# Kernel optimization log

Hardware: AMD Instinct MI355X
Metric: run time of the kernel (lower is better)

Reference implementation:

```python
import jax, jax.numpy as jnp
import numpy as np

B, L, D, H = 8, 1024, 512, 8
DH = D // H
DF = 2048


def setup_inputs() -> dict:
    key = jax.random.key(0)
    ks = jax.random.split(key, 13)
    s = 0.02
    return {
        "hid": jax.random.normal(ks[0], (B, L, D), jnp.float32),
        "img": jax.random.normal(ks[1], (B, L, D), jnp.float32),
        "Wq": s * jax.random.normal(ks[2], (D, D), jnp.float32),
        "Wk": s * jax.random.normal(ks[3], (D, D), jnp.float32),
        "Wv": s * jax.random.normal(ks[4], (D, D), jnp.float32),
        "Wo": s * jax.random.normal(ks[5], (D, D), jnp.float32),
        "Wq2": s * jax.random.normal(ks[6], (D, D), jnp.float32),
        "Wk2": s * jax.random.normal(ks[7], (D, D), jnp.float32),
        "Wv2": s * jax.random.normal(ks[8], (D, D), jnp.float32),
        "Wo2": s * jax.random.normal(ks[9], (D, D), jnp.float32),
        "W1": s * jax.random.normal(ks[10], (D, DF), jnp.float32),
        "W2": s * jax.random.normal(ks[11], (DF, D), jnp.float32),
        "seq": jax.random.randint(ks[12], (B, L), 0, 4),
        "SOC": 3,
        "EOS": 100,
    }


def _ln(x):
    mu = x.mean(-1, keepdims=True)
    v = x.var(-1, keepdims=True)
    return (x - mu) * jax.lax.rsqrt(v + 1e-5)


def _attn(q_in, k_in, v_in, Wq, Wk, Wv, Wo, key_mask=None):
    b, lq, _ = q_in.shape
    q = (q_in @ Wq).reshape(b, lq, H, DH)
    k = (k_in @ Wk).reshape(b, -1, H, DH)
    v = (v_in @ Wv).reshape(b, -1, H, DH)
    scores = jnp.einsum('bqhd,bkhd->bhqk', q, k) * (1.0 / np.sqrt(DH))
    if key_mask is not None:
        scores = jnp.where(key_mask[:, None, None, :], scores, jnp.float32(-1e9))
    a = jax.nn.softmax(scores, axis=-1)
    o = jnp.einsum('bhqk,bkhd->bqhd', a, v).reshape(b, lq, D)
    return o @ Wo


def reference(hid, img, Wq, Wk, Wv, Wo, Wq2, Wk2, Wv2, Wo2, W1, W2, seq, SOC, EOS):
    # cell-start mask: SOC tokens before the first EOS
    soc = (seq == SOC) & (jnp.cumsum(seq == EOS, axis=1) == 0)  # [B,L]
    # stable compaction: True positions first, original order preserved
    order = jnp.argsort(~soc, axis=1, stable=True)              # [B,L]
    ext = jnp.take_along_axis(hid, order[:, :, None], axis=1)   # [B,L,D]
    counts = soc.sum(axis=1)                                    # [B]
    run = jnp.arange(L)[None, :] < counts[:, None]              # [B,L] = extract(soc, soc)
    ext = jnp.where(run[:, :, None], ext, 0.0)                  # zero padding rows (F.pad)
    # Blocks: pre-LN masked self-attn + cross-attn to img + FFN
    x = ext
    xn = _ln(x)
    x = x + _attn(xn, xn, xn, Wq, Wk, Wv, Wo, key_mask=run)
    x = x + _attn(_ln(x), img, img, Wq2, Wk2, Wv2, Wo2)
    x = x + jax.nn.gelu(_ln(x) @ W1) @ W2
    # masked_scatter: write the first `count` rows of x back at soc positions, in order
    inv = jnp.argsort(order, axis=1)
    back = jnp.take_along_axis(x, inv[:, :, None], axis=1)
    hid_new = jnp.where(soc[:, :, None], back, hid)
    return (hid_new, x)
```

## Files before the change

kernel.cpp:

```cpp
#include <hip/hip_runtime.h>
#include <cmath>

#define B 8
#define L 1024
#define D 512
#define H 8
#define DH 64
#define DF 2048
#define BLD (B*L*D)
#define M_TOT (B*L)

typedef __attribute__((ext_vector_type(8))) short bf16x8;
typedef __attribute__((ext_vector_type(4))) float f32x4;
typedef const __attribute__((address_space(1))) void* gas_ptr;
typedef __attribute__((address_space(3))) void* las_ptr;

__device__ __forceinline__ unsigned short f2bf(float f) {
    unsigned int u = __builtin_bit_cast(unsigned int, f);
    u += 0x7FFFu + ((u >> 16) & 1u);
    return (unsigned short)(u >> 16);
}
__device__ __forceinline__ float bf2f(unsigned short s) {
    return __builtin_bit_cast(float, ((unsigned int)s) << 16);
}

__device__ __forceinline__ float gelu_f(float x) {
    float x3 = x * x * x;
    return 0.5f * x * (1.0f + tanhf(0.7978845608028654f * (x + 0.044715f * x3)));
}

__global__ __launch_bounds__(1024) void pos_kernel(const int* __restrict__ seq,
                                                   const int* __restrict__ pSOC,
                                                   const int* __restrict__ pEOS,
                                                   int* __restrict__ pos,
                                                   int* __restrict__ counts) {
    int b = blockIdx.x, t = threadIdx.x;
    int lane = t & 63, w = t >> 6;
    int sv = seq[b * L + t];
    int SOC = pSOC[0], EOS = pEOS[0];
    int eosf = (sv == EOS) ? 1 : 0;
    unsigned long long em = __ballot(eosf);
    int eexcl = __popcll(em & ((1ull << lane) - 1ull));
    __shared__ int ewt[16], swt[16];
    if (lane == 63) ewt[w] = eexcl + eosf;
    __syncthreads();
    int ebase = 0;
    for (int i = 0; i < w; ++i) ebase += ewt[i];
    int ecum_incl = ebase + eexcl + eosf;
    int socf = (sv == SOC && ecum_incl == 0) ? 1 : 0;
    unsigned long long sm = __ballot(socf);
    int sexcl = __popcll(sm & ((1ull << lane) - 1ull));
    if (lane == 63) swt[w] = sexcl + socf;
    __syncthreads();
    int sbase = 0, stot = 0;
    for (int i = 0; i < 16; ++i) { int v = swt[i]; if (i < w) sbase += v; stot += v; }
    if (socf) pos[b * L + sbase + sexcl] = t;
    if (t == 0) counts[b] = stot;
}

__global__ void gather_kernel(const float* __restrict__ hid, const int* __restrict__ pos,
                              const int* __restrict__ counts, float* __restrict__ x) {
    int j = blockIdx.x % L, b = blockIdx.x / L;
    int t = threadIdx.x;
    float4 val = make_float4(0.f, 0.f, 0.f, 0.f);
    if (j < counts[b]) {
        const float4* src = (const float4*)(hid + (size_t)(b * L + pos[b * L + j]) * D);
        val = src[t];
    }
    ((float4*)(x + (size_t)(b * L + j) * D))[t] = val;
}

__global__ void scatter_kernel(const float* __restrict__ x, const int* __restrict__ pos,
                               const int* __restrict__ counts, float* __restrict__ out0) {
    int j = blockIdx.x % L, b = blockIdx.x / L;
    if (j >= counts[b]) return;
    int t = threadIdx.x;
    const float4* src = (const float4*)(x + (size_t)(b * L + j) * D);
    float4* dst = (float4*)(out0 + (size_t)(b * L + pos[b * L + j]) * D);
    dst[t] = src[t];
}

__global__ void bcast_kernel(float* __restrict__ x, const int* __restrict__ counts) {
    int j = blockIdx.x % L, b = blockIdx.x / L;
    int cnt = counts[b];
    if (j <= cnt) return;
    int t = threadIdx.x;
    const float4* src = (const float4*)(x + (size_t)(b * L + cnt) * D);
    float4* dst = (float4*)(x + (size_t)(b * L + j) * D);
    dst[t] = src[t];
}

__global__ void ln_kernel(const float* __restrict__ X, unsigned short* __restrict__ Y,
                          const int* __restrict__ counts) {
    int row = blockIdx.x;
    if ((row & 1023 & ~127) > counts[row >> 10]) return;
    int t = threadIdx.x;
    const float* xr = X + (size_t)row * D;
    float a = xr[t], b2 = xr[t + 256];
    float s = a + b2, sq = a * a + b2 * b2;
    for (int m = 1; m < 64; m <<= 1) {
        s += __shfl_xor(s, m);
        sq += __shfl_xor(sq, m);
    }
    __shared__ float ws[4], wq[4];
    int wid = t >> 6;
    if ((t & 63) == 0) { ws[wid] = s; wq[wid] = sq; }
    __syncthreads();
    s = ws[0] + ws[1] + ws[2] + ws[3];
    sq = wq[0] + wq[1] + wq[2] + wq[3];
    float mu = s * (1.0f / D);
    float var = sq * (1.0f / D) - mu * mu;
    float rs = rsqrtf(var + 1e-5f);
    Y[(size_t)row * D + t] = f2bf((a - mu) * rs);
    Y[(size_t)row * D + t + 256] = f2bf((b2 - mu) * rs);
}

struct WtArgs {
    const float* src[10];
    unsigned short* dst[10];
};
__global__ void wtrans_all(WtArgs a) {
    __shared__ float t[32][33];
    int bid = blockIdx.x;
    int w, tn, tk, K, N;
    if (bid < 2048)      { w = bid >> 8;      int t2 = bid & 255;  N = 512;  K = 512;  tn = t2 & 15; tk = t2 >> 4; }
    else if (bid < 3072) { w = 8;             int t2 = bid - 2048; N = 2048; K = 512;  tn = t2 & 63; tk = t2 >> 6; }
    else                 { w = 9;             int t2 = bid - 3072; N = 512;  K = 2048; tn = t2 & 15; tk = t2 >> 4; }
    const float* W = a.src[w];
    unsigned short* Wt = a.dst[w];
    int k0 = tk * 32, n0 = tn * 32;
    int tx = threadIdx.x, ty = threadIdx.y;
    for (int i = ty; i < 32; i += 8)
        t[i][tx] = W[(size_t)(k0 + i) * N + n0 + tx];
    __syncthreads();
    for (int i = ty; i < 32; i += 8)
        Wt[(size_t)(n0 + i) * K + k0 + tx] = f2bf(t[tx][i]);
}

__global__ void cvt_kernel(const float* __restrict__ X, unsigned short* __restrict__ Y, int n4) {
    int i = blockIdx.x * blockDim.x + threadIdx.x;
    if (i >= n4) return;
    float4 f = ((const float4*)X)[i];
    ushort4 u;
    u.x = f2bf(f.x); u.y = f2bf(f.y); u.z = f2bf(f.z); u.w = f2bf(f.w);
    ((ushort4*)Y)[i] = u;
}

template<bool SKIP>
__global__ __launch_bounds__(256) void vtrans_kernel(const unsigned short* __restrict__ V,
                                                     int vstride,
                                                     unsigned short* __restrict__ Vt,
                                                     const int* __restrict__ counts) {
    __shared__ unsigned short t[64][72];
    int l0 = (blockIdx.x & 15) * 64;
    int h = (blockIdx.x >> 4) & 7;
    int b = blockIdx.x >> 7;
    if (SKIP && l0 > counts[b]) return;
    int tid = threadIdx.x;
    const unsigned short* vb = V + (size_t)b * L * vstride + h * DH;
    for (int e = tid; e < 512; e += 256) {
        int i = e >> 3, d0 = (e & 7) * 8;
        *(bf16x8*)&t[i][d0] = *(const bf16x8*)&vb[(size_t)(l0 + i) * vstride + d0];
    }
    __syncthreads();
    for (int e = tid; e < 512; e += 256) {
        int d = e & 63, i0 = (e >> 6) * 8;
        bf16x8 val;
        #pragma unroll
        for (int j = 0; j < 8; ++j) val[j] = t[i0 + j][d];
        *(bf16x8*)&Vt[((size_t)((b * H + h) * DH + d)) * L + l0 + i0] = val;
    }
}

template<int MODE, bool SKIP, int S>
__global__ __launch_bounds__(256) void gemm_mfma(const unsigned short* __restrict__ A,
                                                 const unsigned short* __restrict__ Wt,
                                                 void* __restrict__ Cv,
                                                 int K, int N,
                                                 const int* __restrict__ counts) {
    int m0 = blockIdx.y * 64, n0 = blockIdx.x * 128;
    if (SKIP && (m0 & 1023) > counts[m0 >> 10]) return;
    int Kc = K / S;
    int kbeg = blockIdx.z * Kc;
    int nk = Kc / 64;
    __shared__ __align__(16) unsigned short As[3][64 * 64];
    __shared__ __align__(16) unsigned short Bs[3][128 * 64];
    int tid = threadIdx.x, lane = tid & 63, wid = tid >> 6;
    int wm = (wid >> 1) * 32, wn = (wid & 1) * 64;
    int r16 = lane & 15, g = lane >> 4;
    f32x4 acc[2][4] = {};

#define STAGE(bufi, kt) do {                                                          \
    int kk_ = kbeg + (kt) * 64;                                                       \
    _Pragma("unroll")                                                                 \
    for (int q_ = 0; q_ < 2; ++q_) {                                                  \
        int e_ = q_ * 256 + tid;                                                      \
        int r_ = e_ >> 3, c_ = ((e_ & 7) ^ (r_ & 7)) * 8;                             \
        __builtin_amdgcn_global_load_lds((gas_ptr)(A + (size_t)(m0 + r_) * K + kk_ + c_), \
                                         (las_ptr)(&As[bufi][0] + (size_t)e_ * 8), 16, 0, 0); \
    }                                                                                 \
    _Pragma("unroll")                                                                 \
    for (int q_ = 0; q_ < 4; ++q_) {                                                  \
        int e_ = q_ * 256 + tid;                                                      \
        int r_ = e_ >> 3, c_ = ((e_ & 7) ^ (r_ & 7)) * 8;                             \
        __builtin_amdgcn_global_load_lds((gas_ptr)(Wt + (size_t)(n0 + r_) * K + kk_ + c_), \
                                         (las_ptr)(&Bs[bufi][0] + (size_t)e_ * 8), 16, 0, 0); \
    }                                                                                 \
} while (0)

    STAGE(0, 0);
    if (nk > 1) STAGE(1, 1);
    asm volatile("s_waitcnt vmcnt(6)" ::: "memory");
    __builtin_amdgcn_s_barrier();
    __builtin_amdgcn_sched_barrier(0);
    int swz = (r16 & 7) * 8;
    for (int kt = 0; kt < nk; ++kt) {
        int cur = kt % 3;
        if (kt + 2 < nk) STAGE((kt + 2) % 3, kt + 2);
        #pragma unroll
        for (int ks = 0; ks < 2; ++ks) {
            bf16x8 av[2], bv[4];
            #pragma unroll
            for (int m = 0; m < 2; ++m)
                av[m] = *(const bf16x8*)&As[cur][(wm + m * 16 + r16) * 64 + ((ks * 32 + g * 8) ^ swz)];
            #pragma unroll
            for (int n = 0; n < 4; ++n)
                bv[n] = *(const bf16x8*)&Bs[cur][(wn + n * 16 + r16) * 64 + ((ks * 32 + g * 8) ^ swz)];
            #pragma unroll
            for (int m = 0; m < 2; ++m)
                #pragma unroll
                for (int n = 0; n < 4; ++n)
                    acc[m][n] = __builtin_amdgcn_mfma_f32_16x16x32_bf16(av[m], bv[n], acc[m][n], 0, 0, 0);
        }
        if (kt + 2 < nk) asm volatile("s_waitcnt vmcnt(6)" ::: "memory");
        else             asm volatile("s_waitcnt vmcnt(0)" ::: "memory");
        __builtin_amdgcn_s_barrier();
        __builtin_amdgcn_sched_barrier(0);
    }
#undef STAGE
    #pragma unroll
    for (int m = 0; m < 2; ++m)
        #pragma unroll
        for (int n = 0; n < 4; ++n)
            #pragma unroll
            for (int r = 0; r < 4; ++r) {
                int grow = m0 + wm + m * 16 + g * 4 + r;
                int gcol = n0 + wn + n * 16 + r16;
                size_t off = (size_t)grow * N + gcol;
                float vv = acc[m][n][r];
                if (MODE == 1) {
                    if (S > 1) atomicAdd((float*)Cv + off, vv);
                    else ((float*)Cv)[off] += vv;
                }
                else if (MODE == 2) ((unsigned short*)Cv)[off] = f2bf(gelu_f(vv));
                else ((unsigned short*)Cv)[off] = f2bf(vv);
            }
}

template<bool MASK, bool SPLIT>
__global__ __launch_bounds__(256) void attn_mfma(const unsigned short* __restrict__ Q, int qstride,
                                                 const unsigned short* __restrict__ Kb, int kstride,
                                                 const unsigned short* __restrict__ Vt,
                                                 unsigned short* __restrict__ O,
                                                 unsigned short* __restrict__ PO,
                                                 float* __restrict__ ML,
                                                 const int* __restrict__ counts) {
    int nwg = gridDim.x;
    int wg = (blockIdx.x & 7) * (nwg >> 3) + (blockIdx.x >> 3);
    int qt = wg & 15;
    int cidx = SPLIT ? ((wg >> 4) & 1) : 0;
    int h = SPLIT ? ((wg >> 5) & 7) : ((wg >> 4) & 7);
    int b = SPLIT ? (wg >> 8) : (wg >> 7);
    int cntb = counts[b];
    if (qt * 64 > cntb) return;
    __shared__ __align__(16) unsigned short Ks[64][64];
    __shared__ __align__(16) unsigned short Vs[64][64];
    __shared__ __align__(16) unsigned short Ps[4][16][64];
    int tid = threadIdx.x, lane = tid & 63, wid = tid >> 6;
    int q0 = qt * 64 + wid * 16;
    int cnt = MASK ? cntb : L;
    int nt = MASK ? min(16, max(1, (cnt + 63) >> 6)) : 16;
    int kt0 = SPLIT ? cidx * 8 : 0;
    int kt1 = SPLIT ? (cidx * 8 + 8) : nt;
    int r16 = lane & 15, g = lane >> 4;
    int swmask = (r16 & 7) << 3;
    const unsigned short* qbase = Q + ((size_t)(b * L + q0 + r16) * qstride + h * DH + g * 8);
    bf16x8 qv0 = *(const bf16x8*)(qbase);
    bf16x8 qv1 = *(const bf16x8*)(qbase + 32);
    f32x4 o_acc[4] = {};
    float m_run[4], l_run[4];
    #pragma unroll
    for (int r = 0; r < 4; ++r) { m_run[r] = -1e30f; l_run[r] = 0.f; }
    const unsigned short* kb = Kb + (size_t)b * L * kstride + h * DH;
    const unsigned short* vtb = Vt + (size_t)(b * H + h) * DH * L;
    bf16x8 kreg[2], vreg[2];
    #pragma unroll
    for (int q = 0; q < 2; ++q) {
        int e = q * 256 + tid, kv = e >> 3, c0 = (e & 7) * 8;
        kreg[q] = *(const bf16x8*)&kb[(size_t)(kt0 * 64 + kv) * kstride + c0];
        vreg[q] = *(const bf16x8*)&vtb[(size_t)kv * L + kt0 * 64 + c0];
    }
    for (int kt = kt0; kt < kt1; ++kt) {
        __syncthreads();
        #pragma unroll
        for (int q = 0; q < 2; ++q) {
            int e = q * 256 + tid, kv = e >> 3, c0 = (e & 7) * 8;
            int sw = c0 ^ ((kv & 7) << 3);
            *(bf16x8*)&Ks[kv][sw] = kreg[q];
            *(bf16x8*)&Vs[kv][sw] = vreg[q];
        }
        __syncthreads();
        if (kt + 1 < kt1) {
            #pragma unroll
            for (int q = 0; q < 2; ++q) {
                int e = q * 256 + tid, kv = e >> 3, c0 = (e & 7) * 8;
                kreg[q] = *(const bf16x8*)&kb[(size_t)((kt + 1) * 64 + kv) * kstride + c0];
                vreg[q] = *(const bf16x8*)&vtb[(size_t)kv * L + (kt + 1) * 64 + c0];
            }
        }
        f32x4 s[4];
        #pragma unroll
        for (int n = 0; n < 4; ++n) {
            bf16x8 k0 = *(const bf16x8*)&Ks[n * 16 + r16][(g * 8) ^ swmask];
            bf16x8 k1 = *(const bf16x8*)&Ks[n * 16 + r16][(g * 8 + 32) ^ swmask];
            f32x4 z = {};
            z = __builtin_amdgcn_mfma_f32_16x16x32_bf16(qv0, k0, z, 0, 0, 0);
            s[n] = __builtin_amdgcn_mfma_f32_16x16x32_bf16(qv1, k1, z, 0, 0, 0);
        }
        #pragma unroll
        for (int n = 0; n < 4; ++n)
            #pragma unroll
            for (int r = 0; r < 4; ++r) {
                float v = s[n][r] * 0.125f;
                if (MASK) {
                    int kidx = kt * 64 + n * 16 + r16;
                    v = (kidx < cnt) ? v : -1e30f;
                }
                s[n][r] = v;
            }
        #pragma unroll
        for (int r = 0; r < 4; ++r) {
            float rm = fmaxf(fmaxf(s[0][r], s[1][r]), fmaxf(s[2][r], s[3][r]));
            #pragma unroll
            for (int mm = 1; mm < 16; mm <<= 1) rm = fmaxf(rm, __shfl_xor(rm, mm));
            float m_new = fmaxf(m_run[r], rm);
            float rs = 0.f;
            #pragma unroll
            for (int n = 0; n < 4; ++n) { float e = __expf(s[n][r] - m_new); s[n][r] = e; rs += e; }
            #pragma unroll
            for (int mm = 1; mm < 16; mm <<= 1) rs += __shfl_xor(rs, mm);
            float factor = __expf(m_run[r] - m_new);
            l_run[r] = l_run[r] * factor + rs;
            m_run[r] = m_new;
            #pragma unroll
            for (int n = 0; n < 4; ++n) o_acc[n][r] *= factor;
        }
        #pragma unroll
        for (int n = 0; n < 4; ++n)
            #pragma unroll
            for (int r = 0; r < 4; ++r) {
                int qrow = g * 4 + r;
                Ps[wid][qrow][(n * 16 + r16) ^ ((qrow & 7) << 3)] = f2bf(s[n][r]);
            }
        bf16x8 pa0 = *(const bf16x8*)&Ps[wid][r16][(g * 8) ^ swmask];
        bf16x8 pa1 = *(const bf16x8*)&Ps[wid][r16][(g * 8 + 32) ^ swmask];
        #pragma unroll
        for (int n = 0; n < 4; ++n) {
            bf16x8 v0 = *(const bf16x8*)&Vs[n * 16 + r16][(g * 8) ^ swmask];
            bf16x8 v1 = *(const bf16x8*)&Vs[n * 16 + r16][(g * 8 + 32) ^ swmask];
            o_acc[n] = __builtin_amdgcn_mfma_f32_16x16x32_bf16(pa0, v0, o_acc[n], 0, 0, 0);
            o_acc[n] = __builtin_amdgcn_mfma_f32_16x16x32_bf16(pa1, v1, o_acc[n], 0, 0, 0);
        }
    }
    #pragma unroll
    for (int r = 0; r < 4; ++r) {
        float inv = 1.0f / l_run[r];
        int row = q0 + g * 4 + r;
        if (SPLIT) {
            size_t basec = (((size_t)cidx * B + b) * H + h) * L + row;
            #pragma unroll
            for (int n = 0; n < 4; ++n)
                PO[basec * DH + n * 16 + r16] = f2bf(o_acc[n][r] * inv);
            if (r16 == 0) { ML[basec * 2] = m_run[r]; ML[basec * 2 + 1] = l_run[r]; }
        } else {
            size_t ro = (size_t)(b * L + row) * D + h * DH;
            #pragma unroll
            for (int n = 0; n < 4; ++n)
                O[ro + n * 16 + r16] = f2bf(o_acc[n][r] * inv);
        }
    }
}

__global__ __launch_bounds__(256) void attn_merge(const unsigned short* __restrict__ PO,
                                                  const float* __restrict__ ML,
                                                  unsigned short* __restrict__ O,
                                                  const int* __restrict__ counts) {
    int qt = blockIdx.x & 15, h = (blockIdx.x >> 4) & 7, b = blockIdx.x >> 7;
    if (qt * 64 > counts[b]) return;
    int tid = threadIdx.x;
    int row = qt * 64 + (tid >> 2);
    int d0 = (tid & 3) * 16;
    size_t base = (size_t)(b * H + h) * L + row;
    size_t cstride = (size_t)B * H * L;
    float m0 = ML[base * 2], l0 = ML[base * 2 + 1];
    float m1 = ML[(base + cstride) * 2], l1 = ML[(base + cstride) * 2 + 1];
    float M = fmaxf(m0, m1);
    float w0 = __expf(m0 - M) * l0, w1 = __expf(m1 - M) * l1;
    float inv = 1.0f / (w0 + w1);
    w0 *= inv; w1 *= inv;
    const bf16x8* p0 = (const bf16x8*)&PO[base * DH + d0];
    const bf16x8* p1 = (const bf16x8*)&PO[(base + cstride) * DH + d0];
    unsigned short* op = O + ((size_t)(b * L + row) * D + h * DH + d0);
    #pragma unroll
    for (int q = 0; q < 2; ++q) {
        bf16x8 a = p0[q], c = p1[q], r;
        #pragma unroll
        for (int j = 0; j < 8; ++j)
            r[j] = (short)f2bf(bf2f((unsigned short)a[j]) * w0 + bf2f((unsigned short)c[j]) * w1);
        *(bf16x8*)(op + q * 8) = r;
    }
}

extern "C" void kernel_launch(void* const* d_in, const int* in_sizes, int n_in,
                              void* d_out, int out_size, void* d_ws, size_t ws_size,
                              hipStream_t stream) {
    const float* hid = (const float*)d_in[0];
    const float* img = (const float*)d_in[1];
    const int* seq   = (const int*)d_in[12];
    const int* pSOC  = (const int*)d_in[13];
    const int* pEOS  = (const int*)d_in[14];
    float* out0 = (float*)d_out;
    float* out1 = out0 + (size_t)BLD;

    char* w = (char*)d_ws;
    int* pos    = (int*)w;
    int* counts = pos + B * L;
    size_t off = 64 * 1024;
    float* x = (float*)(w + off);                     off += (size_t)BLD * 4;
    unsigned short* qkv = (unsigned short*)(w + off); off += (size_t)M_TOT * 3 * D * 2;
    unsigned short* o   = (unsigned short*)(w + off); off += (size_t)BLD * 2;
    unsigned short* vt  = (unsigned short*)(w + off); off += (size_t)BLD * 2;
    unsigned short* xn  = (unsigned short*)(w + off); off += (size_t)BLD * 2;
    unsigned short* imgb= (unsigned short*)(w + off); off += (size_t)BLD * 2;
    unsigned short* Wqt  = (unsigned short*)(w + off); off += (size_t)D * D * 2;
    unsigned short* Wkt  = (unsigned short*)(w + off); off += (size_t)D * D * 2;
    unsigned short* Wvt  = (unsigned short*)(w + off); off += (size_t)D * D * 2;
    unsigned short* Wot  = (unsigned short*)(w + off); off += (size_t)D * D * 2;
    unsigned short* Wq2t = (unsigned short*)(w + off); off += (size_t)D * D * 2;
    unsigned short* Wk2t = (unsigned short*)(w + off); off += (size_t)D * D * 2;
    unsigned short* Wv2t = (unsigned short*)(w + off); off += (size_t)D * D * 2;
    unsigned short* Wo2t = (unsigned short*)(w + off); off += (size_t)D * D * 2;
    unsigned short* W1t  = (unsigned short*)(w + off); off += (size_t)D * DF * 2;
    unsigned short* W2t  = (unsigned short*)(w + off); off += (size_t)D * DF * 2;
    float* ml            = (float*)(w + off);          off += (size_t)2 * B * H * L * 2 * 4;
    unsigned short* q2  = qkv;
    unsigned short* kv2 = qkv + (size_t)M_TOT * D;
    unsigned short* mid = qkv;
    unsigned short* po  = xn;

    pos_kernel<<<B, 1024, 0, stream>>>(seq, pSOC, pEOS, pos, counts);
    WtArgs wa;
    wa.src[0] = (const float*)d_in[2];  wa.dst[0] = Wqt;
    wa.src[1] = (const float*)d_in[3];  wa.dst[1] = Wkt;
    wa.src[2] = (const float*)d_in[4];  wa.dst[2] = Wvt;
    wa.src[3] = (const float*)d_in[5];  wa.dst[3] = Wot;
    wa.src[4] = (const float*)d_in[6];  wa.dst[4] = Wq2t;
    wa.src[5] = (const float*)d_in[7];  wa.dst[5] = Wk2t;
    wa.src[6] = (const float*)d_in[8];  wa.dst[6] = Wv2t;
    wa.src[7] = (const float*)d_in[9];  wa.dst[7] = Wo2t;
    wa.src[8] = (const float*)d_in[10]; wa.dst[8] = W1t;
    wa.src[9] = (const float*)d_in[11]; wa.dst[9] = W2t;
    wtrans_all<<<4096, dim3(32, 8), 0, stream>>>(wa);
    cvt_kernel<<<(BLD / 4 + 255) / 256, 256, 0, stream>>>(img, imgb, BLD / 4);

    gather_kernel<<<B * L, 128, 0, stream>>>(hid, pos, counts, x);

    int attn_grid = B * H * (L / 64);
    ln_kernel<<<M_TOT, 256, 0, stream>>>(x, xn, counts);
    gemm_mfma<3, true, 1><<<dim3(12, 128, 1), 256, 0, stream>>>(xn, Wqt, qkv, D, 3 * D, counts);
    vtrans_kernel<true><<<attn_grid, 256, 0, stream>>>(qkv + 2 * D, 3 * D, vt, counts);
    attn_mfma<true, false><<<attn_grid, 256, 0, stream>>>(qkv, 3 * D, qkv + D, 3 * D, vt, o, po, ml, counts);
    gemm_mfma<1, true, 4><<<dim3(4, 128, 4), 256, 0, stream>>>(o, Wot, x, D, D, counts);
    ln_kernel<<<M_TOT, 256, 0, stream>>>(x, xn, counts);
    gemm_mfma<3, false, 1><<<dim3(8, 128, 1), 256, 0, stream>>>(imgb, Wk2t, kv2, D, 2 * D, counts);
    gemm_mfma<3, true, 1><<<dim3(4, 128, 1), 256, 0, stream>>>(xn, Wq2t, q2, D, D, counts);
    vtrans_kernel<false><<<attn_grid, 256, 0, stream>>>(kv2 + D, 2 * D, vt, counts);
    attn_mfma<false, true><<<attn_grid * 2, 256, 0, stream>>>(q2, D, kv2, 2 * D, vt, o, po, ml, counts);
    attn_merge<<<attn_grid, 256, 0, stream>>>(po, ml, o, counts);
    gemm_mfma<1, true, 4><<<dim3(4, 128, 4), 256, 0, stream>>>(o, Wo2t, x, D, D, counts);
    ln_kernel<<<M_TOT, 256, 0, stream>>>(x, xn, counts);
    gemm_mfma<2, true, 1><<<dim3(16, 128, 1), 256, 0, stream>>>(xn, W1t, mid, D, DF, counts);
    gemm_mfma<1, true, 4><<<dim3(4, 128, 4), 256, 0, stream>>>(mid, W2t, x, DF, D, counts);
    bcast_kernel<<<B * L, 128, 0, stream>>>(x, counts);
    hipMemcpyAsync(out0, hid, (size_t)BLD * sizeof(float), hipMemcpyDeviceToDevice, stream);
    hipMemcpyAsync(out1, x, (size_t)BLD * sizeof(float), hipMemcpyDeviceToDevice, stream);
    scatter_kernel<<<B * L, 128, 0, stream>>>(x, pos, counts, out0);
}
```

Baseline: 246.5 us.

## Fuse gather with layernorm, merge output epilogue, add 128x128 GEMM tiles

Gather of cell-start rows is fused with the first layernorm, so the compacted rows are not re-read. The image bf16 conversion is folded into the weight-transpose launch. The broadcast, two device memcpys and the scatter are replaced by one epilogue kernel that uses a new inverse-rank map to write both outputs directly. A new 128x128-tile MFMA GEMM is used for the QKV, cross KV and both FFN projections, trading more LDS and registers for more data reuse per tile.

Measured after the change: 232.8 us, median of 3. 5.5% less time.

```diff
diff --git a/kernel.cpp b/kernel.cpp
--- a/kernel.cpp
+++ b/kernel.cpp
@@ -33,6 +33,7 @@
                                                    const int* __restrict__ pSOC,
                                                    const int* __restrict__ pEOS,
                                                    int* __restrict__ pos,
+                                                   int* __restrict__ inv,
                                                    int* __restrict__ counts) {
     int b = blockIdx.x, t = threadIdx.x;
     int lane = t & 63, w = t >> 6;
@@ -54,40 +55,58 @@
     __syncthreads();
     int sbase = 0, stot = 0;
     for (int i = 0; i < 16; ++i) { int v = swt[i]; if (i < w) sbase += v; stot += v; }
-    if (socf) pos[b * L + sbase + sexcl] = t;
+    int rank = sbase + sexcl;
+    if (socf) pos[b * L + rank] = t;
+    inv[b * L + t] = socf ? rank : -1;
     if (t == 0) counts[b] = stot;
 }
 
-__global__ void gather_kernel(const float* __restrict__ hid, const int* __restrict__ pos,
-                              const int* __restrict__ counts, float* __restrict__ x) {
-    int j = blockIdx.x % L, b = blockIdx.x / L;
-    int t = threadIdx.x;
-    float4 val = make_float4(0.f, 0.f, 0.f, 0.f);
-    if (j < counts[b]) {
-        const float4* src = (const float4*)(hid + (size_t)(b * L + pos[b * L + j]) * D);
-        val = src[t];
-    }
-    ((float4*)(x + (size_t)(b * L + j) * D))[t] = val;
-}
-
-__global__ void scatter_kernel(const float* __restrict__ x, const int* __restrict__ pos,
-                               const int* __restrict__ counts, float* __restrict__ out0) {
-    int j = blockIdx.x % L, b = blockIdx.x / L;
-    if (j >= counts[b]) return;
-    int t = threadIdx.x;
-    const float4* src = (const float4*)(x + (size_t)(b * L + j) * D);
-    float4* dst = (float4*)(out0 + (size_t)(b * L + pos[b * L + j]) * D);
-    dst[t] = src[t];
-}
-
-__global__ void bcast_kernel(float* __restrict__ x, const int* __restrict__ counts) {
+__global__ void gather_ln(const float* __restrict__ hid, const int* __restrict__ pos,
+                          const int* __restrict__ counts,
+                          float* __restrict__ X, unsigned short* __restrict__ Y) {
     int j = blockIdx.x % L, b = blockIdx.x / L;
     int cnt = counts[b];
-    if (j <= cnt) return;
+    if ((j & ~127) > cnt) return;
     int t = threadIdx.x;
-    const float4* src = (const float4*)(x + (size_t)(b * L + cnt) * D);
-    float4* dst = (float4*)(x + (size_t)(b * L + j) * D);
-    dst[t] = src[t];
+    float a = 0.f, b2 = 0.f;
+    if (j < cnt) {
+        const float* src = hid + (size_t)(b * L + pos[b * L + j]) * D;
+        a = src[t]; b2 = src[t + 256];
+    }
+    size_t row = (size_t)(b * L + j);
+    X[row * D + t] = a;
+    X[row * D + t + 256] = b2;
+    float s = a + b2, sq = a * a + b2 * b2;
+    for (int m = 1; m < 64; m <<= 1) {
+        s += __shfl_xor(s, m);
+        sq += __shfl_xor(sq, m);
+    }
+    __shared__ float ws[4], wq[4];
+    int wid = t >> 6;
+    if ((t & 63) == 0) { ws[wid] = s; wq[wid] = sq; }
+    __syncthreads();
+    s = ws[0] + ws[1] + ws[2] + ws[3];
+    sq = wq[0] + wq[1] + wq[2] + wq[3];
+    float mu = s * (1.0f / D);
+    float var = sq * (1.0f / D) - mu * mu;
+    float rs = rsqrtf(var + 1e-5f);
+    Y[row * D + t] = f2bf((a - mu) * rs);
+    Y[row * D + t + 256] = f2bf((b2 - mu) * rs);
+}
+
+__global__ void epilogue_kernel(const float* __restrict__ x, const float* __restrict__ hid,
+                                const int* __restrict__ inv, const int* __restrict__ counts,
+                                float* __restrict__ out0, float* __restrict__ out1) {
+    int l = blockIdx.x % L, b = blockIdx.x / L;
+    int t = threadIdx.x;
+    int cnt = counts[b];
+    int r = inv[b * L + l];
+    const float4* s0 = (const float4*)((r >= 0 ? x + (size_t)(b * L + r) * D
+                                               : hid + (size_t)(b * L + l) * D));
+    ((float4*)(out0 + (size_t)(b * L + l) * D))[t] = s0[t];
+    int jsrc = l < cnt ? l : cnt;
+    const float4* s1 = (const float4*)(x + (size_t)(b * L + jsrc) * D);
+    ((float4*)(out1 + (size_t)(b * L + l) * D))[t] = s1[t];
 }
 
 __global__ void ln_kernel(const float* __restrict__ X, unsigned short* __restrict__ Y,
@@ -118,10 +137,22 @@
 struct WtArgs {
     const float* src[10];
     unsigned short* dst[10];
+    const float* img;
+    unsigned short* imgb;
 };
-__global__ void wtrans_all(WtArgs a) {
+__global__ void wtrans_cvt_all(WtArgs a) {
+    int bid = blockIdx.x;
+    int tx = threadIdx.x, ty = threadIdx.y;
+    if (bid >= 4096) {
+        int t = ty * 32 + tx;
+        int i = (bid - 4096) * 256 + t;
+        float4 f = ((const float4*)a.img)[i];
+        ushort4 u;
+        u.x = f2bf(f.x); u.y = f2bf(f.y); u.z = f2bf(f.z); u.w = f2bf(f.w);
+        ((ushort4*)a.imgb)[i] = u;
+        return;
+    }
     __shared__ float t[32][33];
-    int bid = blockIdx.x;
     int w, tn, tk, K, N;
     if (bid < 2048)      { w = bid >> 8;      int t2 = bid & 255;  N = 512;  K = 512;  tn = t2 & 15; tk = t2 >> 4; }
     else if (bid < 3072) { w = 8;             int t2 = bid - 2048; N = 2048; K = 512;  tn = t2 & 63; tk = t2 >> 6; }
@@ -129,21 +160,11 @@
     const float* W = a.src[w];
     unsigned short* Wt = a.dst[w];
     int k0 = tk * 32, n0 = tn * 32;
-    int tx = threadIdx.x, ty = threadIdx.y;
     for (int i = ty; i < 32; i += 8)
         t[i][tx] = W[(size_t)(k0 + i) * N + n0 + tx];
     __syncthreads();
     for (int i = ty; i < 32; i += 8)
         Wt[(size_t)(n0 + i) * K + k0 + tx] = f2bf(t[tx][i]);
-}
-
-__global__ void cvt_kernel(const float* __restrict__ X, unsigned short* __restrict__ Y, int n4) {
-    int i = blockIdx.x * blockDim.x + threadIdx.x;
-    if (i >= n4) return;
-    float4 f = ((const float4*)X)[i];
-    ushort4 u;
-    u.x = f2bf(f.x); u.y = f2bf(f.y); u.z = f2bf(f.z); u.w = f2bf(f.w);
-    ((ushort4*)Y)[i] = u;
 }
 
 template<bool SKIP>
@@ -240,6 +261,89 @@
 #undef STAGE
     #pragma unroll
     for (int m = 0; m < 2; ++m)
+        #pragma unroll
+        for (int n = 0; n < 4; ++n)
+            #pragma unroll
+            for (int r = 0; r < 4; ++r) {
+                int grow = m0 + wm + m * 16 + g * 4 + r;
+                int gcol = n0 + wn + n * 16 + r16;
+                size_t off = (size_t)grow * N + gcol;
+                float vv = acc[m][n][r];
+                if (MODE == 1) {
+                    if (S > 1) atomicAdd((float*)Cv + off, vv);
+                    else ((float*)Cv)[off] += vv;
+                }
+                else if (MODE == 2) ((unsigned short*)Cv)[off] = f2bf(gelu_f(vv));
+                else ((unsigned short*)Cv)[off] = f2bf(vv);
+            }
+}
+
+template<int MODE, bool SKIP, int S>
+__global__ __launch_bounds__(256) void gemm_mfma128(const unsigned short* __restrict__ A,
+                                                    const unsigned short* __restrict__ Wt,
+                                                    void* __restrict__ Cv,
+                                                    int K, int N,
+                                                    const int* __restrict__ counts) {
+    int m0 = blockIdx.y * 128, n0 = blockIdx.x * 128;
+    if (SKIP && (m0 & 1023) > counts[m0 >> 10]) return;
+    int Kc = K / S;
+    int kbeg = blockIdx.z * Kc;
+    int nk = Kc / 64;
+    __shared__ __align__(16) unsigned short As[2][128 * 64];
+    __shared__ __align__(16) unsigned short Bs[2][128 * 64];
+    int tid = threadIdx.x, lane = tid & 63, wid = tid >> 6;
+    int wm = (wid >> 1) * 64, wn = (wid & 1) * 64;
+    int r16 = lane & 15, g = lane >> 4;
+    f32x4 acc[4][4] = {};
+
+#define STAGE(bufi, kt) do {                                                          \
+    int kk_ = kbeg + (kt) * 64;                                                       \
+    _Pragma("unroll")                                                                 \
+    for (int q_ = 0; q_ < 4; ++q_) {                                                  \
+        int e_ = q_ * 256 + tid;                                                      \
+        int r_ = e_ >> 3, c_ = ((e_ & 7) ^ (r_ & 7)) * 8;                             \
+        __builtin_amdgcn_global_load_lds((gas_ptr)(A + (size_t)(m0 + r_) * K + kk_ + c_), \
+                                         (las_ptr)(&As[bufi][0] + (size_t)e_ * 8), 16, 0, 0); \
+        __builtin_amdgcn_global_load_lds((gas_ptr)(Wt + (size_t)(n0 + r_) * K + kk_ + c_), \
+                                         (las_ptr)(&Bs[bufi][0] + (size_t)e_ * 8), 16, 0, 0); \
+    }                                                                                 \
+} while (0)
+
+    STAGE(0, 0);
+    if (nk > 1) STAGE(1, 1);
+    asm volatile("s_waitcnt vmcnt(8)" ::: "memory");
+    __builtin_amdgcn_s_barrier();
+    __builtin_amdgcn_sched_barrier(0);
+    int swz = (r16 & 7) * 8;
+    for (int kt = 0; kt < nk; ++kt) {
+        int cur = kt & 1;
+        #pragma unroll
+        for (int ks = 0; ks < 2; ++ks) {
+            bf16x8 av[4], bv[4];
+            #pragma unroll
+            for (int m = 0; m < 4; ++m)
+                av[m] = *(const bf16x8*)&As[cur][(wm + m * 16 + r16) * 64 + ((ks * 32 + g * 8) ^ swz)];
+            #pragma unroll
+            for (int n = 0; n < 4; ++n)
+                bv[n] = *(const bf16x8*)&Bs[cur][(wn + n * 16 + r16) * 64 + ((ks * 32 + g * 8) ^ swz)];
+            #pragma unroll
+            for (int m = 0; m < 4; ++m)
+                #pragma unroll
+                for (int n = 0; n < 4; ++n)
+                    acc[m][n] = __builtin_amdgcn_mfma_f32_16x16x32_bf16(av[m], bv[n], acc[m][n], 0, 0, 0);
+        }
+        __builtin_amdgcn_s_barrier();
+        if (kt + 2 < nk) STAGE(cur, kt + 2);
+        if (kt + 1 < nk) {
+            if (kt + 2 < nk) asm volatile("s_waitcnt vmcnt(8)" ::: "memory");
+            else             asm volatile("s_waitcnt vmcnt(0)" ::: "memory");
+        }
+        __builtin_amdgcn_s_barrier();
+        __builtin_amdgcn_sched_barrier(0);
+    }
+#undef STAGE
+    #pragma unroll
+    for (int m = 0; m < 4; ++m)
         #pragma unroll
         for (int n = 0; n < 4; ++n)
             #pragma unroll
@@ -434,8 +538,9 @@
 
     char* w = (char*)d_ws;
     int* pos    = (int*)w;
-    int* counts = pos + B * L;
-    size_t off = 64 * 1024;
+    int* inv    = pos + B * L;
+    int* counts = inv + B * L;
+    size_t off = 128 * 1024;
     float* x = (float*)(w + off);                     off += (size_t)BLD * 4;
     unsigned short* qkv = (unsigned short*)(w + off); off += (size_t)M_TOT * 3 * D * 2;
     unsigned short* o   = (unsigned short*)(w + off); off += (size_t)BLD * 2;
@@ -458,7 +563,7 @@
     unsigned short* mid = qkv;
     unsigned short* po  = xn;
 
-    pos_kernel<<<B, 1024, 0, stream>>>(seq, pSOC, pEOS, pos, counts);
+    pos_kernel<<<B, 1024, 0, stream>>>(seq, pSOC, pEOS, pos, inv, counts);
     WtArgs wa;
     wa.src[0] = (const float*)d_in[2];  wa.dst[0] = Wqt;
     wa.src[1] = (const float*)d_in[3];  wa.dst[1] = Wkt;
@@ -470,29 +575,24 @@
     wa.src[7] = (const float*)d_in[9];  wa.dst[7] = Wo2t;
     wa.src[8] = (const float*)d_in[10]; wa.dst[8] = W1t;
     wa.src[9] = (const float*)d_in[11]; wa.dst[9] = W2t;
-    wtrans_all<<<4096, dim3(32, 8), 0, stream>>>(wa);
-    cvt_kernel<<<(BLD / 4 + 255) / 256, 256, 0, stream>>>(img, imgb, BLD / 4);
-
-    gather_kernel<<<B * L, 128, 0, stream>>>(hid, pos, counts, x);
+    wa.img = img; wa.imgb = imgb;
+    wtrans_cvt_all<<<8192, dim3(32, 8), 0, stream>>>(wa);
 
     int attn_grid = B * H * (L / 64);
-    ln_kernel<<<M_TOT, 256, 0, stream>>>(x, xn, counts);
-    gemm_mfma<3, true, 1><<<dim3(12, 128, 1), 256, 0, stream>>>(xn, Wqt, qkv, D, 3 * D, counts);
+    gather_ln<<<B * L, 256, 0, stream>>>(hid, pos, counts, x, xn);
+    gemm_mfma128<3, true, 1><<<dim3(12, 64, 1), 256, 0, stream>>>(xn, Wqt, qkv, D, 3 * D, counts);
     vtrans_kernel<true><<<attn_grid, 256, 0, stream>>>(qkv + 2 * D, 3 * D, vt, counts);
     attn_mfma<true, false><<<attn_grid, 256, 0, stream>>>(qkv, 3 * D, qkv + D, 3 * D, vt, o, po, ml, counts);
     gemm_mfma<1, true, 4><<<dim3(4, 128, 4), 256, 0, stream>>>(o, Wot, x, D, D, counts);
     ln_kernel<<<M_TOT, 256, 0, stream>>>(x, xn, counts);
-    gemm_mfma<3, false, 1><<<dim3(8, 128, 1), 256, 0, stream>>>(imgb, Wk2t, kv2, D, 2 * D, counts);
+    gemm_mfma128<3, false, 1><<<dim3(8, 64, 1), 256, 0, stream>>>(imgb, Wk2t, kv2, D, 2 * D, counts);
     gemm_mfma<3, true, 1><<<dim3(4, 128, 1), 256, 0, stream>>>(xn, Wq2t, q2, D, D, counts);
     vtrans_kernel<false><<<attn_grid, 256, 0, stream>>>(kv2 + D, 2 * D, vt, counts);
     attn_mfma<false, true><<<attn_grid * 2, 256, 0, stream>>>(q2, D, kv2, 2 * D, vt, o, po, ml, counts);
     attn_merge<<<attn_grid, 256, 0, stream>>>(po, ml, o, counts);
     gemm_mfma<1, true, 4><<<dim3(4, 128, 4), 256, 0, stream>>>(o, Wo2t, x, D, D, counts);
     ln_kernel<<<M_TOT, 256, 0, stream>>>(x, xn, counts);
-    gemm_mfma<2, true, 1><<<dim3(16, 128, 1), 256, 0, stream>>>(xn, W1t, mid, D, DF, counts);
-    gemm_mfma<1, true, 4><<<dim3(4, 128, 4), 256, 0, stream>>>(mid, W2t, x, DF, D, counts);
-    bcast_kernel<<<B * L, 128, 0, stream>>>(x, counts);
-    hipMemcpyAsync(out0, hid, (size_t)BLD * sizeof(float), hipMemcpyDeviceToDevice, stream);
-    hipMemcpyAsync(out1, x, (size_t)BLD * sizeof(float), hipMemcpyDeviceToDevice, stream);
-    scatter_kernel<<<B * L, 128, 0, stream>>>(x, pos, counts, out0);
-}
+    gemm_mfma128<2, true, 1><<<dim3(16, 64, 1), 256, 0, stream>>>(xn, W1t, mid, D, DF, counts);
+    gemm_mfma128<1, true, 4><<<dim3(4, 64, 4), 256, 0, stream>>>(mid, W2t, x, DF, D, counts);
+    epilogue_kernel<<<B * L, 128, 0, stream>>>(x, hid, inv, counts, out0, out1);
+}
```
